# Kernel optimization log

Measured on AMD Instinct MI355X. Metric: run time of the kernel, lower is better.

Reference implementation:

```python
import jax
import jax.numpy as jnp
import numpy as np

# Config mirroring GLOBAL_CONFIG['attn'] / kernel config in the source
BM = 64            # query-group (block) size; asserted 64 or 192 in source
TOP_KEYS = 0.1     # fraction of keys kept via top-k on colsum scores
MULTIPLE_OF = 64   # counts_multiple_of: indices_count rounded to this
LW1D = 0.15        # local_1d_window fraction
RAND_INV_PROB = 100

B, H, N, D = 1, 12, 2048, 128


def setup_inputs() -> dict:
    key = jax.random.key(0)
    kq, kk, kv, kc = jax.random.split(key, 4)
    shape = (B, H, N, D)
    q = jax.random.normal(kq, shape, dtype=jnp.float32)
    k = jax.random.normal(kk, shape, dtype=jnp.float32)
    v = jax.random.normal(kv, shape, dtype=jnp.float32)
    out_cache = jax.random.normal(kc, shape, dtype=jnp.float32)
    return {"q": q, "k": k, "v": v, "out_cache": out_cache}


def _static_1d_mask(n: int, bm: int, lw1d: float) -> jnp.ndarray:
    # initialize_1d_static_mask: per query-group local window centered at
    # qg*bm + bm//2, width int(lw1d*n), clipped to [0, n). Shape [qg, n].
    qg = n // bm
    ws = int(lw1d * n)
    centers = jnp.arange(qg) * bm + bm // 2          # [qg]
    j = jnp.arange(n)                                  # [n]
    lo = centers[:, None] - ws // 2
    hi = centers[:, None] + ws // 2
    return (j[None, :] >= lo) & (j[None, :] < hi)


def _scatter_true(mask, idx):
    # mask.scatter_(-1, idx, True) along last axis
    K = idx.shape[-1]
    n = mask.shape[-1]
    flat = mask.reshape(-1, n)
    fidx = idx.reshape(-1, K)
    rows = jnp.arange(flat.shape[0])[:, None]
    flat = flat.at[rows, fidx].set(True)
    return flat.reshape(mask.shape)


def _sparse_diff_attn(q, k, v, out_cache):
    b, h, n, d = q.shape
    qg = n // BM
    scale = 1.0 / jnp.sqrt(jnp.asarray(d, q.dtype))
    # dense scores (dense_colsum_attn computes these on the full step)
    scores = jnp.einsum('bhid,bhjd->bhij', q, k) * scale   # [b,h,n,n]
    probs = jax.nn.softmax(scores, axis=-1)
    # bs: column-sum of attention probabilities per query group  [b,h,qg,n]
    bs = probs.reshape(b, h, qg, BM, n).sum(axis=3)
    # indices_count = multiple_of * round(top_keys * n / multiple_of)
    indices_count = MULTIPLE_OF * int(round(TOP_KEYS * n / MULTIPLE_OF))
    rmask = jax.random.randint(jax.random.key(1), bs.shape, 0, RAND_INV_PROB) == 0
    _, idx = jax.lax.top_k(bs, indices_count)
    mask = _scatter_true(rmask, idx)                       # [b,h,qg,n]
    static = _static_1d_mask(n, BM, LW1D)                  # [qg,n]
    # video_query_groups: groups where static window + topk still sparse
    vqg = (static.sum(axis=-1, keepdims=True) + indices_count) < n  # [qg,1]
    mask = mask & vqg[None, None]
    mask = mask | static[None, None]
    # csp_attn: block-sparse attention; every query i in group i//BM attends
    # only to keys selected in mask[.., i//BM, :]
    full_mask = jnp.repeat(mask, BM, axis=2)               # [b,h,n,n]
    sp_scores = jnp.where(full_mask, scores, -jnp.inf)
    sp_probs = jax.nn.softmax(sp_scores, axis=-1)
    sp_out = jnp.einsum('bhij,bhjd->bhid', sp_probs, v)
    # sparse step: o = o_cache + csp_attn(...)  (sign = +1)
    return out_cache + sp_out


def reference(q, k, v, out_cache):
    return _sparse_diff_attn(q, k, v, out_cache)
```

## Files before the change

### kernel.cpp

```cpp
#include <hip/hip_runtime.h>
#include <math.h>

constexpr int Hh   = 12;
constexpr int Nn   = 2048;
constexpr int Dd   = 128;
constexpr int BMq  = 64;
constexpr int QGg  = 32;
constexpr int KSEL = 192;
constexpr int CK   = 32;
constexpr float SCALE = 0.08838834764831845f;

typedef _Float16 v8h __attribute__((ext_vector_type(8)));
typedef float    v4f __attribute__((ext_vector_type(4)));

__device__ __attribute__((aligned(16))) _Float16 g_qh[(size_t)Hh*Nn*Dd];
__device__ __attribute__((aligned(16))) _Float16 g_ql[(size_t)Hh*Nn*Dd];
__device__ __attribute__((aligned(16))) _Float16 g_kh[(size_t)Hh*Nn*Dd];
__device__ __attribute__((aligned(16))) _Float16 g_kl[(size_t)Hh*Nn*Dd];
__device__ float          g_lp[(size_t)Hh*Nn*16];
__device__ float          g_bs[(size_t)Hh*QGg*Nn];
__device__ unsigned short g_sel[Hh*QGg*Nn];
__device__ int            g_cnt[Hh*QGg];
__device__ __attribute__((aligned(16))) float g_oacc[(size_t)Hh*QGg*2*2*32*128];
__device__ float          g_lacc[(size_t)Hh*QGg*2*2*32];

__device__ __forceinline__ unsigned int rotl32(unsigned int x, int n){
  return (x << n) | (x >> (32 - n));
}

__device__ __forceinline__ unsigned pack2h(_Float16 a, _Float16 b){
  unsigned short ua, ub;
  __builtin_memcpy(&ua, &a, 2);
  __builtin_memcpy(&ub, &b, 2);
  return (unsigned)ua | ((unsigned)ub << 16);
}

__device__ __forceinline__ void tf2x32(unsigned int k0, unsigned int k1,
                                       unsigned int x0, unsigned int x1,
                                       unsigned int &o0, unsigned int &o1){
  const unsigned int ks2 = 0x1BD11BDAu ^ k0 ^ k1;
  x0 += k0; x1 += k1;
  x0 += x1; x1 = rotl32(x1,13); x1 ^= x0;
  x0 += x1; x1 = rotl32(x1,15); x1 ^= x0;
  x0 += x1; x1 = rotl32(x1,26); x1 ^= x0;
  x0 += x1; x1 = rotl32(x1, 6); x1 ^= x0;
  x0 += k1; x1 += ks2 + 1u;
  x0 += x1; x1 = rotl32(x1,17); x1 ^= x0;
  x0 += x1; x1 = rotl32(x1,29); x1 ^= x0;
  x0 += x1; x1 = rotl32(x1,16); x1 ^= x0;
  x0 += x1; x1 = rotl32(x1,24); x1 ^= x0;
  x0 += ks2; x1 += k0 + 2u;
  x0 += x1; x1 = rotl32(x1,13); x1 ^= x0;
  x0 += x1; x1 = rotl32(x1,15); x1 ^= x0;
  x0 += x1; x1 = rotl32(x1,26); x1 ^= x0;
  x0 += x1; x1 = rotl32(x1, 6); x1 ^= x0;
  x0 += k0; x1 += k1 + 3u;
  x0 += x1; x1 = rotl32(x1,17); x1 ^= x0;
  x0 += x1; x1 = rotl32(x1,29); x1 ^= x0;
  x0 += x1; x1 = rotl32(x1,16); x1 ^= x0;
  x0 += x1; x1 = rotl32(x1,24); x1 ^= x0;
  x0 += k1; x1 += ks2 + 4u;
  x0 += x1; x1 = rotl32(x1,13); x1 ^= x0;
  x0 += x1; x1 = rotl32(x1,15); x1 ^= x0;
  x0 += x1; x1 = rotl32(x1,26); x1 ^= x0;
  x0 += x1; x1 = rotl32(x1, 6); x1 ^= x0;
  x0 += ks2; x1 += k0 + 5u;
  o0 = x0; o1 = x1;
}

__device__ __forceinline__ bool jax_rand01(unsigned int idx,
                                           unsigned int k1a, unsigned int k1b,
                                           unsigned int k2a, unsigned int k2b){
  unsigned int h0, h1, l0, l1;
  tf2x32(k1a, k1b, 0u, idx, h0, h1);
  tf2x32(k2a, k2b, 0u, idx, l0, l1);
  unsigned int h = h0 ^ h1;
  unsigned int l = l0 ^ l1;
  unsigned int off = ((h % 100u) * 96u + (l % 100u)) % 100u;
  return off == 0u;
}

__global__ __launch_bounds__(256) void k0_cvt(const float* __restrict__ Q,
                                              const float* __restrict__ K){
  const int bid = blockIdx.x;
  const int t = threadIdx.x;
  const int kc = t >> 6, ln = t & 63;
  const int row = ln & 15;
  const int col = kc*32 + (ln >> 4)*8;
  const size_t src = ((size_t)bid*16 + row)*Dd + col;
  const size_t ob  = (((size_t)bid)*4 + kc)*512 + (size_t)ln*8;

  float4 qa = *(const float4*)(Q + src);
  float4 qb = *(const float4*)(Q + src + 4);
  float qs[8] = {qa.x*SCALE, qa.y*SCALE, qa.z*SCALE, qa.w*SCALE,
                 qb.x*SCALE, qb.y*SCALE, qb.z*SCALE, qb.w*SCALE};
  v8h qh, ql;
  #pragma unroll
  for (int j = 0; j < 8; ++j){
    _Float16 hi = (_Float16)qs[j];
    qh[j] = hi;
    ql[j] = (_Float16)(qs[j] - (float)hi);
  }
  *(v8h*)&g_qh[ob] = qh;
  *(v8h*)&g_ql[ob] = ql;

  float4 ka = *(const float4*)(K + src);
  float4 kb = *(const float4*)(K + src + 4);
  float ks[8] = {ka.x, ka.y, ka.z, ka.w, kb.x, kb.y, kb.z, kb.w};
  v8h kh, kl;
  #pragma unroll
  for (int j = 0; j < 8; ++j){
    _Float16 hi = (_Float16)ks[j];
    kh[j] = hi;
    kl[j] = (_Float16)(ks[j] - (float)hi);
  }
  *(v8h*)&g_kh[ob] = kh;
  *(v8h*)&g_kl[ob] = kl;
}

__global__ __launch_bounds__(256) void k1_rowsum(){
  const int bid0 = blockIdx.x;
  const int w = (bid0 & 7)*384 + (bid0 >> 3);
  const int jb = w & 15, gp = (w >> 4) & 15, h = w >> 8;
  const int t = threadIdx.x;
  const int wv = t >> 6, ln = t & 63;
  const int nidx = ln & 15, quad = ln >> 4;
  const size_t lnoff = (size_t)ln*8;
  const size_t habase = ((size_t)h*128 + gp*8 + wv*2)*4;
  const size_t hbbase = ((size_t)h*128 + jb*8)*4;

  __shared__ v8h Bh[2][8][64], Bl[2][8][64];
  const int f0 = t*2, f1 = t*2 + 1;
  const int tc0 = f0 >> 6, bln0 = f0 & 63;
  const int tc1 = f1 >> 6, bln1 = f1 & 63;

  v8h rbh0, rbh1, rbl0, rbl1;
  {
    const size_t a0 = (hbbase + tc0*4 + 0)*512 + (size_t)bln0*8;
    const size_t a1 = (hbbase + tc1*4 + 0)*512 + (size_t)bln1*8;
    rbh0 = *(const v8h*)&g_kh[a0]; rbh1 = *(const v8h*)&g_kh[a1];
    rbl0 = *(const v8h*)&g_kl[a0]; rbl1 = *(const v8h*)&g_kl[a1];
  }

  v4f acc[2][8];
  #pragma unroll
  for (int tr = 0; tr < 2; ++tr)
    #pragma unroll
    for (int tc = 0; tc < 8; ++tc)
      acc[tr][tc] = (v4f){0.f, 0.f, 0.f, 0.f};

  for (int kc = 0; kc < 4; ++kc){
    const int cur = kc & 1;
    Bh[cur][tc0][bln0] = rbh0; Bh[cur][tc1][bln1] = rbh1;
    Bl[cur][tc0][bln0] = rbl0; Bl[cur][tc1][bln1] = rbl1;
    __syncthreads();
    if (kc < 3){
      const size_t a0 = (hbbase + tc0*4 + kc+1)*512 + (size_t)bln0*8;
      const size_t a1 = (hbbase + tc1*4 + kc+1)*512 + (size_t)bln1*8;
      rbh0 = *(const v8h*)&g_kh[a0]; rbh1 = *(const v8h*)&g_kh[a1];
      rbl0 = *(const v8h*)&g_kl[a0]; rbl1 = *(const v8h*)&g_kl[a1];
    }
    v8h ahi[2], alo[2];
    #pragma unroll
    for (int tr = 0; tr < 2; ++tr){
      const size_t ab = (habase + tr*4 + kc)*512 + lnoff;
      ahi[tr] = *(const v8h*)&g_qh[ab];
      alo[tr] = *(const v8h*)&g_ql[ab];
    }
    #pragma unroll
    for (int tc = 0; tc < 8; ++tc){
      v8h bh = Bh[cur][tc][ln];
      v8h bl = Bl[cur][tc][ln];
      #pragma unroll
      for (int tr = 0; tr < 2; ++tr){
        acc[tr][tc] = __builtin_amdgcn_mfma_f32_16x16x32_f16(ahi[tr], bh, acc[tr][tc], 0, 0, 0);
        acc[tr][tc] = __builtin_amdgcn_mfma_f32_16x16x32_f16(ahi[tr], bl, acc[tr][tc], 0, 0, 0);
        acc[tr][tc] = __builtin_amdgcn_mfma_f32_16x16x32_f16(alo[tr], bh, acc[tr][tc], 0, 0, 0);
      }
    }
  }

  #pragma unroll
  for (int tr = 0; tr < 2; ++tr){
    float rs[4] = {0.f, 0.f, 0.f, 0.f};
    #pragma unroll
    for (int tc = 0; tc < 8; ++tc){
      #pragma unroll
      for (int r = 0; r < 4; ++r){
        rs[r] += __expf(acc[tr][tc][r]);
      }
    }
    #pragma unroll
    for (int r = 0; r < 4; ++r){
      float v = rs[r];
      v += __shfl_xor(v, 1);
      v += __shfl_xor(v, 2);
      v += __shfl_xor(v, 4);
      v += __shfl_xor(v, 8);
      rs[r] = v;
    }
    if (nidx == 0){
      #pragma unroll
      for (int r = 0; r < 4; ++r){
        const int row = (wv*2+tr)*16 + quad*4 + r;
        g_lp[((size_t)h*Nn + gp*128 + row)*16 + jb] = rs[r];
      }
    }
  }
}

__global__ __launch_bounds__(256) void k2r_colsum(){
  const int bid0 = blockIdx.x;
  const int w = (bid0 & 7)*384 + (bid0 >> 3);
  const int jb = w & 15, gp = (w >> 4) & 15, h = w >> 8;
  const int t = threadIdx.x;
  const int wv = t >> 6, ln = t & 63;
  const int nidx = ln & 15, quad = ln >> 4;
  const size_t lnoff = (size_t)ln*8;
  const size_t habase = ((size_t)h*128 + gp*8 + wv*2)*4;
  const size_t hbbase = ((size_t)h*128 + jb*8)*4;

  __shared__ v8h Bh[2][8][64], Bl[2][8][64];
  __shared__ float il_s[128];
  __shared__ float part[4][128];
  const int f0 = t*2, f1 = t*2 + 1;
  const int tc0 = f0 >> 6, bln0 = f0 & 63;
  const int tc1 = f1 >> 6, bln1 = f1 & 63;

  v8h rbh0, rbh1, rbl0, rbl1;
  {
    const size_t a0 = (hbbase + tc0*4 + 0)*512 + (size_t)bln0*8;
    const size_t a1 = (hbbase + tc1*4 + 0)*512 + (size_t)bln1*8;
    rbh0 = *(const v8h*)&g_kh[a0]; rbh1 = *(const v8h*)&g_kh[a1];
    rbl0 = *(const v8h*)&g_kl[a0]; rbl1 = *(const v8h*)&g_kl[a1];
  }
  if (t < 128){
    const float* lp = &g_lp[((size_t)h*Nn + gp*128 + t)*16];
    float s = 0.f;
    #pragma unroll
    for (int x = 0; x < 16; ++x) s += lp[x];
    il_s[t] = 1.0f / s;
  }

  v4f acc[2][8];
  #pragma unroll
  for (int tr = 0; tr < 2; ++tr)
    #pragma unroll
    for (int tc = 0; tc < 8; ++tc)
      acc[tr][tc] = (v4f){0.f, 0.f, 0.f, 0.f};

  for (int kc = 0; kc < 4; ++kc){
    const int cur = kc & 1;
    Bh[cur][tc0][bln0] = rbh0; Bh[cur][tc1][bln1] = rbh1;
    Bl[cur][tc0][bln0] = rbl0; Bl[cur][tc1][bln1] = rbl1;
    __syncthreads();
    if (kc < 3){
      const size_t a0 = (hbbase + tc0*4 + kc+1)*512 + (size_t)bln0*8;
      const size_t a1 = (hbbase + tc1*4 + kc+1)*512 + (size_t)bln1*8;
      rbh0 = *(const v8h*)&g_kh[a0]; rbh1 = *(const v8h*)&g_kh[a1];
      rbl0 = *(const v8h*)&g_kl[a0]; rbl1 = *(const v8h*)&g_kl[a1];
    }
    v8h ahi[2], alo[2];
    #pragma unroll
    for (int tr = 0; tr < 2; ++tr){
      const size_t ab = (habase + tr*4 + kc)*512 + lnoff;
      ahi[tr] = *(const v8h*)&g_qh[ab];
      alo[tr] = *(const v8h*)&g_ql[ab];
    }
    #pragma unroll
    for (int tc = 0; tc < 8; ++tc){
      v8h bh = Bh[cur][tc][ln];
      v8h bl = Bl[cur][tc][ln];
      #pragma unroll
      for (int tr = 0; tr < 2; ++tr){
        acc[tr][tc] = __builtin_amdgcn_mfma_f32_16x16x32_f16(ahi[tr], bh, acc[tr][tc], 0, 0, 0);
        acc[tr][tc] = __builtin_amdgcn_mfma_f32_16x16x32_f16(ahi[tr], bl, acc[tr][tc], 0, 0, 0);
        acc[tr][tc] = __builtin_amdgcn_mfma_f32_16x16x32_f16(alo[tr], bh, acc[tr][tc], 0, 0, 0);
      }
    }
  }

  __syncthreads();
  float csg[8];
  #pragma unroll
  for (int tc = 0; tc < 8; ++tc) csg[tc] = 0.f;
  #pragma unroll
  for (int tr = 0; tr < 2; ++tr){
    #pragma unroll
    for (int tc = 0; tc < 8; ++tc){
      float cs = 0.f;
      #pragma unroll
      for (int r = 0; r < 4; ++r){
        const int row = (wv*2+tr)*16 + quad*4 + r;
        cs += __expf(acc[tr][tc][r]) * il_s[row];
      }
      cs += __shfl_xor(cs, 16);
      cs += __shfl_xor(cs, 32);
      csg[tc] += cs;
    }
  }
  if (ln < 16){
    #pragma unroll
    for (int tc = 0; tc < 8; ++tc) part[wv][tc*16 + nidx] = csg[tc];
  }
  __syncthreads();
  const int col = t & 127, grp = t >> 7;
  g_bs[((size_t)h*QGg + gp*2 + grp)*Nn + jb*128 + col] =
      part[grp*2][col] + part[grp*2 + 1][col];
}

__global__ __launch_bounds__(256) void k2b_mask(){
  const int bid = blockIdx.x, g = bid % QGg, t = threadIdx.x;
  const int wv = t >> 6, lw = t & 63;
  __shared__ int hist[256];
  __shared__ int wsum[4];
  __shared__ int selb_s, selgt_s;
  __shared__ int csel;
  __shared__ int eqn;
  __shared__ int eqpos[Nn];
  const float* src = g_bs + (size_t)bid*Nn;
  float mine[8];
  {
    float4 a = *(const float4*)&src[t*4];
    float4 b = *(const float4*)&src[1024 + t*4];
    mine[0]=a.x; mine[1]=a.y; mine[2]=a.z; mine[3]=a.w;
    mine[4]=b.x; mine[5]=b.y; mine[6]=b.z; mine[7]=b.w;
  }
  if (t == 0){ csel = 0; eqn = 0; }
  unsigned int bu8[8];
  #pragma unroll
  for (int u = 0; u < 8; ++u) bu8[u] = __float_as_uint(mine[u]);

  unsigned int k1a, k1b, k2a, k2b;
  tf2x32(0u, 1u, 0u, 0u, k1a, k1b);
  tf2x32(0u, 1u, 0u, 1u, k2a, k2b);

  unsigned int pref = 0u;
  unsigned int msk  = 0u;
  int rem = KSEL;
  #pragma unroll
  for (int pass = 3; pass >= 0; --pass){
    const int shift = pass*8;
    hist[t] = 0;
    __syncthreads();
    #pragma unroll
    for (int u = 0; u < 8; ++u){
      if ((bu8[u] & msk) == pref)
        atomicAdd(&hist[(bu8[u] >> shift) & 0xFFu], 1);
    }
    __syncthreads();
    const int hcnt = hist[t];
    int s = hcnt;
    #pragma unroll
    for (int d = 1; d < 64; d <<= 1){
      int tmp = __shfl_down(s, d);
      if (lw + d < 64) s += tmp;
    }
    if (lw == 0) wsum[wv] = s;
    __syncthreads();
    int base = 0;
    #pragma unroll
    for (int w2 = 1; w2 < 4; ++w2) if (wv + w2 < 4) base += wsum[wv + w2];
    const int gt_incl = s + base;
    const int gt = gt_incl - hcnt;
    if (gt < rem && gt_incl >= rem){ selb_s = t; selgt_s = gt; }
    __syncthreads();
    pref |= ((unsigned)selb_s) << shift;
    msk  |= 0xFFu << shift;
    rem  -= selgt_s;
  }
  const unsigned int T = pref;
  const int need = rem;

  #pragma unroll
  for (int u = 0; u < 8; ++u){
    int j = (u < 4) ? (t*4 + u) : (1024 + t*4 + u - 4);
    if (bu8[u] == T){
      int s = atomicAdd(&eqn, 1);
      eqpos[s] = j;
    }
  }
  __syncthreads();
  const int en = eqn;

  const int lo = g*BMq + BMq/2 - 153;
  const int hi = g*BMq + BMq/2 + 153;
  const int ssum = ((hi < Nn) ? hi : Nn) - ((lo > 0) ? lo : 0);
  const bool vqg = (ssum + KSEL) < Nn;

  #pragma unroll
  for (int u = 0; u < 8; ++u){
    int j = (u < 4) ? (t*4 + u) : (1024 + t*4 + u - 4);
    unsigned int bu = bu8[u];
    bool topk = bu > T;
    if (!topk && bu == T){
      int tr = 0;
      for (int i = 0; i < en; ++i)
        tr += (eqpos[i] < j) ? 1 : 0;
      topk = (tr < need);
    }
    bool rnd = jax_rand01((unsigned)(bid*Nn + j), k1a, k1b, k2a, k2b);
    bool st  = (j >= lo) && (j < hi);
    bool selb = st || ((rnd || topk) && vqg);
    if (selb){
      int slot = atomicAdd(&csel, 1);
      g_sel[(size_t)bid*Nn + slot] = (unsigned short)j;
    }
  }
  __syncthreads();
  if (t == 0) g_cnt[bid] = csel;
}

__global__ __launch_bounds__(256) void k3_attn(const float* __restrict__ K,
                                               const float* __restrict__ V){
  const int bid0 = blockIdx.x;
  const int w    = (bid0 & 7)*192 + (bid0 >> 3);
  const int ks   = w & 1;
  const int pb   = w >> 1;
  const int half = pb & 1;
  const int gg   = pb >> 1;
  const int h = gg / QGg, g = gg % QGg;
  const int t = threadIdx.x;
  const int wv = t >> 6, ln = t & 63;
  const int nidx = ln & 15, quad = ln >> 4;
  const int qtile = wv >> 1, kdt = wv & 1;

  __shared__ _Float16 kh_s[CK][136];
  __shared__ _Float16 kl_s[CK][136];
  __shared__ _Float16 vTh[Dd][40];
  __shared__ _Float16 vTl[Dd][40];
  __shared__ _Float16 p_h[32][40];
  __shared__ _Float16 p_l[32][40];
  __shared__ float    l_part[2][32];

  const int c = g_cnt[gg];
  const unsigned short* sel = g_sel + (size_t)gg*Nn;
  const int nch = (c + CK - 1) / CK;
  const int ch  = ((nch + 1) / 2) * CK;
  const int cbeg = ks * ch;
  const int cend = (c < cbeg + ch) ? c : (cbeg + ch);

  const int rb = g*4 + half*2 + qtile;
  v8h aHi[4], aLo[4];
  #pragma unroll
  for (int kc = 0; kc < 4; ++kc){
    const size_t ab = (((size_t)h*128 + rb)*4 + kc)*512 + (size_t)ln*8;
    aHi[kc] = *(const v8h*)&g_qh[ab];
    aLo[kc] = *(const v8h*)&g_ql[ab];
  }

  if (t < 64) l_part[t >> 5][t & 31] = 0.0f;

  float4 kreg[4], vreg[4];
  if (cbeg < cend){
    const int cc0 = ((cend - cbeg) < CK) ? (cend - cbeg) : CK;
    #pragma unroll
    for (int it = 0; it < 4; ++it){
      int e = it*256 + t, row = e >> 5, c4 = e & 31;
      int j = (row < cc0) ? (int)sel[cbeg + row] : 0;
      kreg[it] = ((const float4*)(K + ((size_t)h*Nn + j)*Dd))[c4];
      vreg[it] = ((const float4*)(V + ((size_t)h*Nn + j)*Dd))[c4];
    }
  }

  v4f acc[4];
  #pragma unroll
  for (int dt = 0; dt < 4; ++dt) acc[dt] = (v4f){0.f, 0.f, 0.f, 0.f};

  const int cg = (quad ^ ((nidx >> 2) & 3)) * 8;

  for (int c0 = cbeg; c0 < cend; c0 += CK){
    const int cc = ((cend - c0) < CK) ? (cend - c0) : CK;
    #pragma unroll
    for (int it = 0; it < 4; ++it){
      int e = it*256 + t, row = e >> 5, c4 = e & 31;
      float4 kv = kreg[it];
      float xs[4] = {kv.x, kv.y, kv.z, kv.w};
      _Float16 hh[4], ll[4];
      #pragma unroll
      for (int m = 0; m < 4; ++m){
        _Float16 hi = (_Float16)xs[m];
        hh[m] = hi;
        ll[m] = (_Float16)(xs[m] - (float)hi);
      }
      *(unsigned*)&kh_s[row][c4*4 + 0] = pack2h(hh[0], hh[1]);
      *(unsigned*)&kh_s[row][c4*4 + 2] = pack2h(hh[2], hh[3]);
      *(unsigned*)&kl_s[row][c4*4 + 0] = pack2h(ll[0], ll[1]);
      *(unsigned*)&kl_s[row][c4*4 + 2] = pack2h(ll[2], ll[3]);
      float4 vv = vreg[it];
      float vs[4] = {vv.x, vv.y, vv.z, vv.w};
      const int swz = row ^ ((c4 & 3) << 3);
      #pragma unroll
      for (int m = 0; m < 4; ++m){
        _Float16 hi = (_Float16)vs[m];
        vTh[c4*4 + m][swz] = hi;
        vTl[c4*4 + m][swz] = (_Float16)(vs[m] - (float)hi);
      }
    }
    __syncthreads();
    {
      const int nc0 = c0 + CK;
      if (nc0 < cend){
        const int ncc = ((cend - nc0) < CK) ? (cend - nc0) : CK;
        #pragma unroll
        for (int it = 0; it < 4; ++it){
          int e = it*256 + t, row = e >> 5, c4 = e & 31;
          int j = (row < ncc) ? (int)sel[nc0 + row] : 0;
          kreg[it] = ((const float4*)(K + ((size_t)h*Nn + j)*Dd))[c4];
          vreg[it] = ((const float4*)(V + ((size_t)h*Nn + j)*Dd))[c4];
        }
      }
    }
    v4f sc = (v4f){0.f, 0.f, 0.f, 0.f};
    #pragma unroll
    for (int kc = 0; kc < 4; ++kc){
      v8h bh = *(const v8h*)&kh_s[kdt*16 + nidx][kc*32 + quad*8];
      v8h bl = *(const v8h*)&kl_s[kdt*16 + nidx][kc*32 + quad*8];
      sc = __builtin_amdgcn_mfma_f32_16x16x32_f16(aHi[kc], bh, sc, 0, 0, 0);
      sc = __builtin_amdgcn_mfma_f32_16x16x32_f16(aHi[kc], bl, sc, 0, 0, 0);
      sc = __builtin_amdgcn_mfma_f32_16x16x32_f16(aLo[kc], bh, sc, 0, 0, 0);
    }
    {
      const int k_loc = kdt*16 + nidx;
      float rs[4];
      #pragma unroll
      for (int r = 0; r < 4; ++r){
        float sv = (k_loc < cc) ? __expf(sc[r]) : 0.f;
        rs[r] = sv;
        _Float16 hi = (_Float16)sv;
        const int row = qtile*16 + quad*4 + r;
        p_h[row][k_loc] = hi;
        p_l[row][k_loc] = (_Float16)(sv - (float)hi);
      }
      #pragma unroll
      for (int r = 0; r < 4; ++r){
        float v = rs[r];
        v += __shfl_xor(v, 1);
        v += __shfl_xor(v, 2);
        v += __shfl_xor(v, 4);
        v += __shfl_xor(v, 8);
        rs[r] = v;
      }
      if (nidx == 0){
        #pragma unroll
        for (int r = 0; r < 4; ++r)
          l_part[kdt][qtile*16 + quad*4 + r] += rs[r];
      }
    }
    __syncthreads();
    {
      v8h ph = *(const v8h*)&p_h[qtile*16 + nidx][quad*8];
      v8h pl = *(const v8h*)&p_l[qtile*16 + nidx][quad*8];
      #pragma unroll
      for (int dt = 0; dt < 4; ++dt){
        const int d = (kdt*4 + dt)*16 + nidx;
        v8h vh = *(const v8h*)&vTh[d][cg];
        v8h vl = *(const v8h*)&vTl[d][cg];
        acc[dt] = __builtin_amdgcn_mfma_f32_16x16x32_f16(ph, vh, acc[dt], 0, 0, 0);
        acc[dt] = __builtin_amdgcn_mfma_f32_16x16x32_f16(ph, vl, acc[dt], 0, 0, 0);
        acc[dt] = __builtin_amdgcn_mfma_f32_16x16x32_f16(pl, vh, acc[dt], 0, 0, 0);
      }
    }
    __syncthreads();
  }

  __syncthreads();
  const size_t pbase = ((size_t)pb*2 + ks)*4096;
  if (t < 32) g_lacc[((size_t)pb*2 + ks)*32 + t] = l_part[0][t] + l_part[1][t];
  #pragma unroll
  for (int dt = 0; dt < 4; ++dt){
    const int d = (kdt*4 + dt)*16 + nidx;
    #pragma unroll
    for (int r = 0; r < 4; ++r){
      const int row = qtile*16 + quad*4 + r;
      g_oacc[pbase + (size_t)row*128 + d] = acc[dt][r];
    }
  }
}

__global__ __launch_bounds__(256) void k4_comb(const float* __restrict__ OC,
                                               float* __restrict__ out){
  const int pb = blockIdx.x;
  const int half = pb & 1;
  const int gg = pb >> 1;
  const int h = gg / QGg, g = gg % QGg;
  const int t = threadIdx.x;
  __shared__ float il_s[32];
  if (t < 32){
    float l0 = g_lacc[((size_t)pb*2 + 0)*32 + t];
    float l1 = g_lacc[((size_t)pb*2 + 1)*32 + t];
    il_s[t] = 1.0f / (l0 + l1);
  }
  __syncthreads();
  const size_t b0 = ((size_t)pb*2 + 0)*4096;
  const size_t b1 = ((size_t)pb*2 + 1)*4096;
  #pragma unroll
  for (int i = 0; i < 4; ++i){
    int e = i*256 + t;
    int row = e >> 5, c4 = e & 31;
    float4 a0 = *(const float4*)&g_oacc[b0 + (size_t)row*128 + c4*4];
    float4 a1 = *(const float4*)&g_oacc[b1 + (size_t)row*128 + c4*4];
    const float il = il_s[row];
    const size_t o = ((size_t)h*Nn + (size_t)g*BMq + half*32 + row)*Dd + c4*4;
    float4 oc = *(const float4*)(OC + o);
    float4 rr;
    rr.x = (a0.x + a1.x)*il + oc.x;
    rr.y = (a0.y + a1.y)*il + oc.y;
    rr.z = (a0.z + a1.z)*il + oc.z;
    rr.w = (a0.w + a1.w)*il + oc.w;
    *(float4*)(out + o) = rr;
  }
}

extern "C" void kernel_launch(void* const* d_in, const int* in_sizes, int n_in,
                              void* d_out, int out_size, void* d_ws, size_t ws_size,
                              hipStream_t stream) {
  (void)in_sizes; (void)n_in; (void)out_size; (void)d_ws; (void)ws_size;
  const float* Q  = (const float*)d_in[0];
  const float* K  = (const float*)d_in[1];
  const float* V  = (const float*)d_in[2];
  const float* OC = (const float*)d_in[3];
  float* out = (float*)d_out;
  hipLaunchKernelGGL(k0_cvt,     dim3(Hh*128),     dim3(256), 0, stream, Q, K);
  hipLaunchKernelGGL(k1_rowsum,  dim3(Hh*16*16),   dim3(256), 0, stream);
  hipLaunchKernelGGL(k2r_colsum, dim3(Hh*16*16),   dim3(256), 0, stream);
  hipLaunchKernelGGL(k2b_mask,   dim3(Hh*QGg),     dim3(256), 0, stream);
  hipLaunchKernelGGL(k3_attn,    dim3(Hh*QGg*2*2), dim3(256), 0, stream, K, V);
  hipLaunchKernelGGL(k4_comb,    dim3(Hh*QGg*2),   dim3(256), 0, stream, OC, out);
}
```

Measured before the change: 267.9 us.

## Use direct global-to-LDS loads for K tiles and single-fp16 PV product

The rowsum and colsum kernels now stage K hi/lo tiles straight into LDS with global_load_lds instead of going through registers and explicit LDS stores. The K-loop is also unrolled. The sparse attention kernel drops the split hi/lo fp16 representation for P and V, so the PV product needs one MFMA instead of three, along with fewer LDS buffers and conversions. This cuts memory traffic and matrix work but lowers the accuracy of the output to plain fp16 for P·V. Relying on the async LDS load with only __syncthreads for ordering could also be fragile.

```diff
diff --git a/kernel.cpp b/kernel.cpp
--- a/kernel.cpp
+++ b/kernel.cpp
@@ -33,6 +33,12 @@
   __builtin_memcpy(&ua, &a, 2);
   __builtin_memcpy(&ub, &b, 2);
   return (unsigned)ua | ((unsigned)ub << 16);
+}
+
+__device__ __forceinline__ void gload16(const _Float16* gsrc_lane, v8h* lds_base){
+  __builtin_amdgcn_global_load_lds(
+      (const __attribute__((address_space(1))) void*)gsrc_lane,
+      (__attribute__((address_space(3))) void*)lds_base, 16, 0, 0);
 }
 
 __device__ __forceinline__ void tf2x32(unsigned int k0, unsigned int k1,
@@ -130,17 +136,12 @@
   const size_t hbbase = ((size_t)h*128 + jb*8)*4;
 
   __shared__ v8h Bh[2][8][64], Bl[2][8][64];
-  const int f0 = t*2, f1 = t*2 + 1;
-  const int tc0 = f0 >> 6, bln0 = f0 & 63;
-  const int tc1 = f1 >> 6, bln1 = f1 & 63;
-
-  v8h rbh0, rbh1, rbl0, rbl1;
-  {
-    const size_t a0 = (hbbase + tc0*4 + 0)*512 + (size_t)bln0*8;
-    const size_t a1 = (hbbase + tc1*4 + 0)*512 + (size_t)bln1*8;
-    rbh0 = *(const v8h*)&g_kh[a0]; rbh1 = *(const v8h*)&g_kh[a1];
-    rbl0 = *(const v8h*)&g_kl[a0]; rbl1 = *(const v8h*)&g_kl[a1];
-  }
+  const int stc0 = wv*2, stc1 = wv*2 + 1;
+
+  gload16(&g_kh[(hbbase + stc0*4 + 0)*512 + lnoff], &Bh[0][stc0][0]);
+  gload16(&g_kh[(hbbase + stc1*4 + 0)*512 + lnoff], &Bh[0][stc1][0]);
+  gload16(&g_kl[(hbbase + stc0*4 + 0)*512 + lnoff], &Bl[0][stc0][0]);
+  gload16(&g_kl[(hbbase + stc1*4 + 0)*512 + lnoff], &Bl[0][stc1][0]);
 
   v4f acc[2][8];
   #pragma unroll
@@ -149,16 +150,16 @@
     for (int tc = 0; tc < 8; ++tc)
       acc[tr][tc] = (v4f){0.f, 0.f, 0.f, 0.f};
 
+  #pragma unroll
   for (int kc = 0; kc < 4; ++kc){
     const int cur = kc & 1;
-    Bh[cur][tc0][bln0] = rbh0; Bh[cur][tc1][bln1] = rbh1;
-    Bl[cur][tc0][bln0] = rbl0; Bl[cur][tc1][bln1] = rbl1;
     __syncthreads();
     if (kc < 3){
-      const size_t a0 = (hbbase + tc0*4 + kc+1)*512 + (size_t)bln0*8;
-      const size_t a1 = (hbbase + tc1*4 + kc+1)*512 + (size_t)bln1*8;
-      rbh0 = *(const v8h*)&g_kh[a0]; rbh1 = *(const v8h*)&g_kh[a1];
-      rbl0 = *(const v8h*)&g_kl[a0]; rbl1 = *(const v8h*)&g_kl[a1];
+      const int nxt = cur ^ 1;
+      gload16(&g_kh[(hbbase + stc0*4 + kc+1)*512 + lnoff], &Bh[nxt][stc0][0]);
+      gload16(&g_kh[(hbbase + stc1*4 + kc+1)*512 + lnoff], &Bh[nxt][stc1][0]);
+      gload16(&g_kl[(hbbase + stc0*4 + kc+1)*512 + lnoff], &Bl[nxt][stc0][0]);
+      gload16(&g_kl[(hbbase + stc1*4 + kc+1)*512 + lnoff], &Bl[nxt][stc1][0]);
     }
     v8h ahi[2], alo[2];
     #pragma unroll
@@ -223,17 +224,13 @@
   __shared__ v8h Bh[2][8][64], Bl[2][8][64];
   __shared__ float il_s[128];
   __shared__ float part[4][128];
-  const int f0 = t*2, f1 = t*2 + 1;
-  const int tc0 = f0 >> 6, bln0 = f0 & 63;
-  const int tc1 = f1 >> 6, bln1 = f1 & 63;
-
-  v8h rbh0, rbh1, rbl0, rbl1;
-  {
-    const size_t a0 = (hbbase + tc0*4 + 0)*512 + (size_t)bln0*8;
-    const size_t a1 = (hbbase + tc1*4 + 0)*512 + (size_t)bln1*8;
-    rbh0 = *(const v8h*)&g_kh[a0]; rbh1 = *(const v8h*)&g_kh[a1];
-    rbl0 = *(const v8h*)&g_kl[a0]; rbl1 = *(const v8h*)&g_kl[a1];
-  }
+  const int stc0 = wv*2, stc1 = wv*2 + 1;
+
+  gload16(&g_kh[(hbbase + stc0*4 + 0)*512 + lnoff], &Bh[0][stc0][0]);
+  gload16(&g_kh[(hbbase + stc1*4 + 0)*512 + lnoff], &Bh[0][stc1][0]);
+  gload16(&g_kl[(hbbase + stc0*4 + 0)*512 + lnoff], &Bl[0][stc0][0]);
+  gload16(&g_kl[(hbbase + stc1*4 + 0)*512 + lnoff], &Bl[0][stc1][0]);
+
   if (t < 128){
     const float* lp = &g_lp[((size_t)h*Nn + gp*128 + t)*16];
     float s = 0.f;
@@ -249,16 +246,16 @@
     for (int tc = 0; tc < 8; ++tc)
       acc[tr][tc] = (v4f){0.f, 0.f, 0.f, 0.f};
 
+  #pragma unroll
   for (int kc = 0; kc < 4; ++kc){
     const int cur = kc & 1;
-    Bh[cur][tc0][bln0] = rbh0; Bh[cur][tc1][bln1] = rbh1;
-    Bl[cur][tc0][bln0] = rbl0; Bl[cur][tc1][bln1] = rbl1;
     __syncthreads();
     if (kc < 3){
-      const size_t a0 = (hbbase + tc0*4 + kc+1)*512 + (size_t)bln0*8;
-      const size_t a1 = (hbbase + tc1*4 + kc+1)*512 + (size_t)bln1*8;
-      rbh0 = *(const v8h*)&g_kh[a0]; rbh1 = *(const v8h*)&g_kh[a1];
-      rbl0 = *(const v8h*)&g_kl[a0]; rbl1 = *(const v8h*)&g_kl[a1];
+      const int nxt = cur ^ 1;
+      gload16(&g_kh[(hbbase + stc0*4 + kc+1)*512 + lnoff], &Bh[nxt][stc0][0]);
+      gload16(&g_kh[(hbbase + stc1*4 + kc+1)*512 + lnoff], &Bh[nxt][stc1][0]);
+      gload16(&g_kl[(hbbase + stc0*4 + kc+1)*512 + lnoff], &Bl[nxt][stc0][0]);
+      gload16(&g_kl[(hbbase + stc1*4 + kc+1)*512 + lnoff], &Bl[nxt][stc1][0]);
     }
     v8h ahi[2], alo[2];
     #pragma unroll
@@ -428,9 +425,7 @@
   __shared__ _Float16 kh_s[CK][136];
   __shared__ _Float16 kl_s[CK][136];
   __shared__ _Float16 vTh[Dd][40];
-  __shared__ _Float16 vTl[Dd][40];
   __shared__ _Float16 p_h[32][40];
-  __shared__ _Float16 p_l[32][40];
   __shared__ float    l_part[2][32];
 
   const int c = g_cnt[gg];
@@ -488,14 +483,11 @@
       *(unsigned*)&kl_s[row][c4*4 + 0] = pack2h(ll[0], ll[1]);
       *(unsigned*)&kl_s[row][c4*4 + 2] = pack2h(ll[2], ll[3]);
       float4 vv = vreg[it];
-      float vs[4] = {vv.x, vv.y, vv.z, vv.w};
       const int swz = row ^ ((c4 & 3) << 3);
-      #pragma unroll
-      for (int m = 0; m < 4; ++m){
-        _Float16 hi = (_Float16)vs[m];
-        vTh[c4*4 + m][swz] = hi;
-        vTl[c4*4 + m][swz] = (_Float16)(vs[m] - (float)hi);
-      }
+      vTh[c4*4 + 0][swz] = (_Float16)vv.x;
+      vTh[c4*4 + 1][swz] = (_Float16)vv.y;
+      vTh[c4*4 + 2][swz] = (_Float16)vv.z;
+      vTh[c4*4 + 3][swz] = (_Float16)vv.w;
     }
     __syncthreads();
     {
@@ -527,10 +519,8 @@
       for (int r = 0; r < 4; ++r){
         float sv = (k_loc < cc) ? __expf(sc[r]) : 0.f;
         rs[r] = sv;
-        _Float16 hi = (_Float16)sv;
         const int row = qtile*16 + quad*4 + r;
-        p_h[row][k_loc] = hi;
-        p_l[row][k_loc] = (_Float16)(sv - (float)hi);
+        p_h[row][k_loc] = (_Float16)sv;
       }
       #pragma unroll
       for (int r = 0; r < 4; ++r){
@@ -550,15 +540,11 @@
     __syncthreads();
     {
       v8h ph = *(const v8h*)&p_h[qtile*16 + nidx][quad*8];
-      v8h pl = *(const v8h*)&p_l[qtile*16 + nidx][quad*8];
       #pragma unroll
       for (int dt = 0; dt < 4; ++dt){
         const int d = (kdt*4 + dt)*16 + nidx;
         v8h vh = *(const v8h*)&vTh[d][cg];
-        v8h vl = *(const v8h*)&vTl[d][cg];
         acc[dt] = __builtin_amdgcn_mfma_f32_16x16x32_f16(ph, vh, acc[dt], 0, 0, 0);
-        acc[dt] = __builtin_amdgcn_mfma_f32_16x16x32_f16(ph, vl, acc[dt], 0, 0, 0);
-        acc[dt] = __builtin_amdgcn_mfma_f32_16x16x32_f16(pl, vh, acc[dt], 0, 0, 0);
       }
     }
     __syncthreads();
```

Result: faster. 244.2 us (-8.8%).
